# Performance work log

Measured on AMD Instinct MI355X. Metric: run time of the kernel, lower is better.

## Reference

```python
import jax, jax.numpy as jnp
import numpy as np

B, C, H, W = 4, 64, 64, 64  # x shape; mask is (B,1,8H,8W)


def _conv(x, w, pad=0):
    return jax.lax.conv_general_dilated(
        x, w, (1, 1), [(pad, pad), (pad, pad)],
        dimension_numbers=('NCHW', 'OIHW', 'NCHW'))


def _inorm(x, eps=1e-5):  # InstanceNorm2d, affine=False, biased var (torch default)
    mu = x.mean(axis=(2, 3), keepdims=True)
    var = x.var(axis=(2, 3), keepdims=True)
    return (x - mu) * jax.lax.rsqrt(var + eps)


def _forward(x, mask, kconv_w1, kconv_w2, fs_w1, fs_w2, fs_b2, fs_fuse_w):
    b, c, h, w = x.shape
    n = h * w
    # MaxPool2d(8,8) then binarize
    m = jax.lax.reduce_window(mask, -jnp.inf, jax.lax.max,
                              (1, 1, 8, 8), (1, 1, 8, 8), 'VALID')
    m = (m > 0).astype(x.dtype)
    back = 1.0 - m
    # ResidualBlock K_conv (shared for K and Q paths in original code)
    y = jax.nn.relu(_inorm(_conv(x, kconv_w1, pad=1)))
    y = _inorm(_conv(y, kconv_w2, pad=1))
    kx = jax.nn.relu(y + x)
    # L2-normalized K/Q over channel dim
    K = (kx * back).reshape(b, c, n)
    K = K / (jnp.linalg.norm(K, axis=1, keepdims=True) + 1e-8)
    Q = (kx * m).reshape(b, c, n)
    Q = Q / (jnp.linalg.norm(Q, axis=1, keepdims=True) + 1e-8)
    V = (x * back).reshape(b, c, n)
    # cosine-similarity score map, temperature 20
    score = jnp.einsum('bcq,bck->bqk', Q, K) * 20.0  # (b, n_q, n_k)
    qm = m.reshape(b, 1, n)      # query mask (foreground)
    km = back.reshape(b, 1, n)   # key mask (background)
    NEG = -1000000.0
    validx = score + (1.0 - km) * NEG + (1.0 - qm.transpose(0, 2, 1)) * NEG
    att = jax.nn.softmax(validx, axis=-1) * (qm.transpose(0, 2, 1) * km)
    # att_fore[b,c,q] = sum_k V[b,c,k] * att[b,q,k]
    att_fore = jnp.einsum('bck,bqk->bcq', V, att).reshape(b, c, h, w)
    # Fusion_score
    feat1 = _conv(jnp.concatenate([x * m, att_fore * m], axis=1), fs_w1)
    s = jax.nn.sigmoid(_conv(feat1, fs_w2) + fs_b2[None, :, None, None])
    fused = _conv(jnp.concatenate([x * m, att_fore * m * (1.0 - s)], axis=1), fs_fuse_w)
    fs_out = fused * m + x * (1.0 - m)
    out = fs_out * m + x * (1.0 - m)
    # visualization attention mask
    visatt = att.sum(axis=1).reshape(b, 1, h, w)
    attmask = jnp.repeat(jnp.repeat(visatt, 8, axis=2), 8, axis=3)  # nearest upsample x8
    attmask = attmask / attmask.max()
    return out, attmask


def setup_inputs() -> dict:
    key = jax.random.key(0)
    ks = jax.random.split(key, 8)

    def wgt(k, shape, fan_in):
        return jax.random.normal(k, shape, jnp.float32) / np.sqrt(fan_in)

    x = jax.random.normal(ks[0], (B, C, H, W), jnp.float32)
    # sparse foreground mask so maxpool(8x8)>0 yields a mixed fg/bg mask
    mask = (jax.random.uniform(ks[1], (B, 1, H * 8, W * 8)) < 0.01).astype(jnp.float32)
    return dict(
        x=x, mask=mask,
        kconv_w1=wgt(ks[2], (C, C, 3, 3), C * 9),
        kconv_w2=wgt(ks[3], (C, C, 3, 3), C * 9),
        fs_w1=wgt(ks[4], (C, 2 * C, 1, 1), 2 * C),
        fs_w2=wgt(ks[5], (C, C, 1, 1), C),
        fs_b2=jnp.zeros((C,), jnp.float32),
        fs_fuse_w=wgt(ks[6], (C, 2 * C, 1, 1), 2 * C),
    )


def reference(x, mask, kconv_w1, kconv_w2, fs_w1, fs_w2, fs_b2, fs_fuse_w):
    return _forward(x, mask, kconv_w1, kconv_w2, fs_w1, fs_w2, fs_b2, fs_fuse_w)
```

## Files before the change

### kernel.cpp

```cpp
#include <hip/hip_runtime.h>
#include <hip/hip_bf16.h>

typedef __hip_bfloat16 bf16;
typedef __attribute__((ext_vector_type(8))) short short8;
typedef __attribute__((ext_vector_type(4))) float f32x4;
typedef __attribute__((ext_vector_type(16))) float f32x16;

#define BB 4
#define CC 64
#define NN 4096
#define MH 512
#define MW 512
#define LS 72

#define WB_AFC  ((size_t)0)
#define WB_QIX  ((size_t)4325376)
#define WB_KIX  ((size_t)4390912)
#define WB_MFL  ((size_t)4456448)
#define WB_CNT  ((size_t)4472832)
#define WB_VIS  ((size_t)4259840)
#define WB_WT1  ((size_t)4476992)
#define WB_WT2  ((size_t)4550720)
#define WB_WFB  ((size_t)4624448)
#define WB_XT   ((size_t)8388608)
#define WB_KXT  ((size_t)10485760)
#define WB_E    ((size_t)16777216)
#define EB_ELEM ((size_t)16777216)
#define WB_AFCP ((size_t)150994944)
#define WB_DENP ((size_t)184549376)
#define WB_VISP ((size_t)185597952)
#define WB_GST  ((size_t)186122240)

__device__ __forceinline__ float us2f(unsigned short u) { return __uint_as_float(((unsigned)u) << 16); }
__device__ __forceinline__ unsigned short f2bu(float f) {
  bf16 h = __float2bfloat16(f);
  return *(unsigned short*)&h;
}

__global__ __launch_bounds__(256) void k_pre(const float* __restrict__ x,
                                             const float* __restrict__ mask,
                                             const float* __restrict__ w1,
                                             const float* __restrict__ w2,
                                             const float* __restrict__ fw1,
                                             const float* __restrict__ fw2,
                                             const float* __restrict__ fwf,
                                             float* __restrict__ outp,
                                             unsigned short* __restrict__ xt,
                                             unsigned char* __restrict__ mfl,
                                             float* __restrict__ vis,
                                             unsigned int* __restrict__ vmaxb,
                                             unsigned short* __restrict__ wT1,
                                             unsigned short* __restrict__ wT2,
                                             unsigned short* __restrict__ wfb) {
  __shared__ float lx[64][65];
  int t = threadIdx.x;
  if (blockIdx.x < 256) {
    int b = blockIdx.x >> 6, p0 = (blockIdx.x & 63) * 64;
    const float* xb = x + (size_t)b * CC * NN + p0;
    float* ob = outp + (size_t)b * CC * NN + p0;
    for (int idx = t; idx < 4096; idx += 256) {
      int c = idx >> 6, j = idx & 63;
      float v = xb[c * NN + j];
      lx[j][c] = v;
      ob[c * NN + j] = v;
    }
    __syncthreads();
    unsigned short* xo = xt + ((size_t)b * NN + p0) * 64;
    for (int idx = t; idx < 2048; idx += 256) {
      int j = idx >> 5, c2 = (idx & 31) * 2;
      ushort2 w2v;
      w2v.x = f2bu(lx[j][c2]);
      w2v.y = f2bu(lx[j][c2 + 1]);
      *(ushort2*)&xo[j * 64 + c2] = w2v;
    }
  } else {
    int g = (blockIdx.x - 256) * 256 + t;
    int o = g >> 2, sub = g & 3;
    int b = o >> 12, p = o & 4095;
    int py = p >> 6, px = p & 63;
    const float* mb = mask + (size_t)b * MH * MW + (py * 8 + sub * 2) * MW + px * 8;
    float mx = 0.f;
    #pragma unroll
    for (int dy = 0; dy < 2; ++dy) {
      const float4* r4 = (const float4*)(mb + dy * MW);
      float4 a = r4[0], c = r4[1];
      mx = fmaxf(mx, fmaxf(fmaxf(a.x, a.y), fmaxf(a.z, a.w)));
      mx = fmaxf(mx, fmaxf(fmaxf(c.x, c.y), fmaxf(c.z, c.w)));
    }
    mx = fmaxf(mx, __shfl_xor(mx, 1));
    mx = fmaxf(mx, __shfl_xor(mx, 2));
    if (sub == 0) {
      mfl[o] = (mx > 0.f) ? 1 : 0;
      vis[o] = 0.f;
    }
    if (g == 0) vmaxb[0] = 0u;
    if (g < 36864) {
      int tap = g >> 12;
      int rem = g & 4095;
      int co = rem >> 6, ci = rem & 63;
      int src = (co * 64 + ci) * 9 + tap;
      wT1[g] = f2bu(w1[src]);
      wT2[g] = f2bu(w2[src]);
    } else if (g < 57344) {
      int j2 = g - 36864;
      if (j2 < 8192)       wfb[j2] = f2bu(fw1[j2]);
      else if (j2 < 12288) wfb[j2] = f2bu(fw2[j2 - 8192]);
      else                 wfb[j2] = f2bu(fwf[j2 - 12288]);
    }
  }
}

__global__ __launch_bounds__(256) void k_compact(const unsigned char* __restrict__ mfl,
                                                 int* __restrict__ qidx, int* __restrict__ kidx,
                                                 int* __restrict__ nq, int* __restrict__ nk) {
  int b = blockIdx.x;
  __shared__ unsigned char lm[4096];
  int t = threadIdx.x;
  *(uint4*)&lm[t * 16] = *(const uint4*)&mfl[b * NN + t * 16];
  __syncthreads();
  if (t >= 64) return;
  int lane = t;
  int qb = 0, kb = 0;
  #pragma unroll
  for (int it = 0; it < 64; ++it) {
    int p = it * 64 + lane;
    bool f = lm[p] != 0;
    unsigned long long bal = __ballot(f);
    int before = __popcll(bal & ((1ULL << lane) - 1ULL));
    if (f)  qidx[b * NN + qb + before] = p;
    if (!f) kidx[b * NN + kb + (lane - before)] = p;
    int cnt = __popcll(bal);
    qb += cnt; kb += 64 - cnt;
  }
  if (lane == 0) { nq[b] = qb; nk[b] = kb; }
}

template <bool NORM_IN>
__global__ __launch_bounds__(256) void k_convm(const unsigned short* __restrict__ src,
                                               const unsigned short* __restrict__ wT,
                                               const float* __restrict__ insum,
                                               const float* __restrict__ insq,
                                               unsigned short* __restrict__ dst,
                                               float* __restrict__ gsump,
                                               float* __restrict__ gsqp) {
  int b = blockIdx.y;
  int r = blockIdx.x;
  __shared__ unsigned short bx[198 * LS];
  __shared__ float nmean[64], ninv[64];
  int t = threadIdx.x;
  if (NORM_IN) {
    if (t < 64) {
      float s = 0.f, s2v = 0.f;
      #pragma unroll 8
      for (int r2 = 0; r2 < 64; ++r2) {
        s   += insum[((size_t)r2 * BB + b) * 64 + t];
        s2v += insq [((size_t)r2 * BB + b) * 64 + t];
      }
      float m = s * (1.f / NN);
      float v = fmaxf(s2v * (1.f / NN) - m * m, 0.f);
      nmean[t] = m; ninv[t] = rsqrtf(v + 1e-5f);
    }
    __syncthreads();
  }
  const unsigned short* sb = src + (size_t)b * NN * 64;
  for (int idx = t; idx < 198 * 8; idx += 256) {
    int row = idx >> 3, c8 = (idx & 7) * 8;
    int dy = row / 66;
    int cx = row - dy * 66 - 1;
    int rr = r + dy - 1;
    uint4 v = make_uint4(0u, 0u, 0u, 0u);
    if ((unsigned)rr < 64u && (unsigned)cx < 64u) {
      v = *(const uint4*)(sb + ((size_t)(rr * 64 + cx)) * 64 + c8);
      if (NORM_IN) {
        unsigned short* e = (unsigned short*)&v;
        #pragma unroll
        for (int j = 0; j < 8; ++j)
          e[j] = f2bu(fmaxf((us2f(e[j]) - nmean[c8 + j]) * ninv[c8 + j], 0.f));
      }
    }
    *(uint4*)&bx[row * LS + c8] = v;
  }
  __syncthreads();
  int lane = t & 63;
  int quad = lane >> 4, col = lane & 15;
  int qw = (t >> 6) * 16;
  f32x4 acc[4] = {{0.f,0.f,0.f,0.f},{0.f,0.f,0.f,0.f},{0.f,0.f,0.f,0.f},{0.f,0.f,0.f,0.f}};
  #pragma unroll
  for (int tap = 0; tap < 9; ++tap) {
    int dy = tap / 3, dx = tap - dy * 3 - 1;
    const unsigned short* wrow = wT + ((size_t)tap * 64 + qw + col) * 64;
    short8 a0 = *(const short8*)(wrow + quad * 8);
    short8 a1 = *(const short8*)(wrow + 32 + quad * 8);
    int rbase = dy * 66 + dx + 1;
    #pragma unroll
    for (int nt = 0; nt < 4; ++nt) {
      int row = rbase + nt * 16 + col;
      short8 b0 = *(const short8*)&bx[row * LS + quad * 8];
      short8 b1 = *(const short8*)&bx[row * LS + 32 + quad * 8];
      acc[nt] = __builtin_amdgcn_mfma_f32_16x16x32_bf16(a0, b0, acc[nt], 0, 0, 0);
      acc[nt] = __builtin_amdgcn_mfma_f32_16x16x32_bf16(a1, b1, acc[nt], 0, 0, 0);
    }
  }
  #pragma unroll
  for (int rr = 0; rr < 4; ++rr) {
    float s1 = acc[0][rr] + acc[1][rr] + acc[2][rr] + acc[3][rr];
    float s2 = acc[0][rr]*acc[0][rr] + acc[1][rr]*acc[1][rr]
             + acc[2][rr]*acc[2][rr] + acc[3][rr]*acc[3][rr];
    s1 += __shfl_xor(s1, 1); s2 += __shfl_xor(s2, 1);
    s1 += __shfl_xor(s1, 2); s2 += __shfl_xor(s2, 2);
    s1 += __shfl_xor(s1, 4); s2 += __shfl_xor(s2, 4);
    s1 += __shfl_xor(s1, 8); s2 += __shfl_xor(s2, 8);
    if (col == 0) {
      int co = qw + quad * 4 + rr;
      gsump[((size_t)r * BB + b) * 64 + co] = s1;
      gsqp [((size_t)r * BB + b) * 64 + co] = s2;
    }
  }
  __syncthreads();
  #pragma unroll
  for (int nt = 0; nt < 4; ++nt)
    #pragma unroll
    for (int rr = 0; rr < 4; ++rr)
      bx[(nt * 16 + col) * LS + qw + quad * 4 + rr] = f2bu(acc[nt][rr]);
  __syncthreads();
  unsigned short* db = dst + ((size_t)b * NN + r * 64) * 64;
  for (int idx = t; idx < 512; idx += 256) {
    int px = idx >> 3, c8 = (idx & 7) * 8;
    *(uint4*)(db + (size_t)px * 64 + c8) = *(const uint4*)&bx[px * LS + c8];
  }
}

__global__ __launch_bounds__(256) void k_knorm(unsigned short* __restrict__ kxt,
                                               const unsigned short* __restrict__ xt,
                                               const float* __restrict__ gsump,
                                               const float* __restrict__ gsqp) {
  int b = blockIdx.x >> 6;
  int p0 = (blockIdx.x & 63) * 64;
  __shared__ float m2[64], i2[64];
  int t = threadIdx.x;
  if (t < 64) {
    float s = 0.f, s2v = 0.f;
    #pragma unroll 8
    for (int r2 = 0; r2 < 64; ++r2) {
      s   += gsump[((size_t)r2 * BB + b) * 64 + t];
      s2v += gsqp [((size_t)r2 * BB + b) * 64 + t];
    }
    float m = s * (1.f / NN);
    float v = fmaxf(s2v * (1.f / NN) - m * m, 0.f);
    m2[t] = m; i2[t] = rsqrtf(v + 1e-5f);
  }
  __syncthreads();
  int px = t >> 2, c0 = (t & 3) * 16;
  size_t base = ((size_t)b * NN + p0 + px) * 64 + c0;
  unsigned short kv[16], xv[16];
  *(uint4*)&kv[0] = *(const uint4*)(kxt + base);
  *(uint4*)&kv[8] = *(const uint4*)(kxt + base + 8);
  *(uint4*)&xv[0] = *(const uint4*)(xt + base);
  *(uint4*)&xv[8] = *(const uint4*)(xt + base + 8);
  float v[16]; float ss = 0.f;
  #pragma unroll
  for (int j = 0; j < 16; ++j) {
    float f = fmaxf((us2f(kv[j]) - m2[c0 + j]) * i2[c0 + j] + us2f(xv[j]), 0.f);
    v[j] = f; ss += f * f;
  }
  ss += __shfl_xor(ss, 1);
  ss += __shfl_xor(ss, 2);
  float inv = 1.f / (sqrtf(ss) + 1e-8f);
  #pragma unroll
  for (int j = 0; j < 16; ++j) kv[j] = f2bu(v[j] * inv);
  *(uint4*)(kxt + base) = *(const uint4*)&kv[0];
  *(uint4*)(kxt + base + 8) = *(const uint4*)&kv[8];
}

__global__ __launch_bounds__(256) void k_att1(const unsigned short* __restrict__ khat,
                                              const unsigned short* __restrict__ xt,
                                              const int* __restrict__ qidx, const int* __restrict__ kidx,
                                              const int* __restrict__ nqv, const int* __restrict__ nkv,
                                              float* __restrict__ afc_part, float* __restrict__ den_part,
                                              unsigned short* __restrict__ eg) {
  int b = blockIdx.y;
  int nqb = nqv[b], nkb = nkv[b];
  int q0 = (blockIdx.x >> 3) * 64;
  int part = blockIdx.x & 7;
  if (q0 >= nqb) return;
  int ntiles = (nkb + 63) >> 6;
  int nt_blk = (part < ntiles) ? ((ntiles - part + 7) >> 3) : 0;
  int NKP = (nkb + 63) & ~63;
  __shared__ unsigned short lk [64 * LS];
  __shared__ unsigned short lvT[64 * LS];
  __shared__ unsigned short le [64 * LS];
  __shared__ int lidxa[512];
  int t = threadIdx.x;
  int wave = t >> 6, lane = t & 63;
  int l31 = lane & 31, lhi = lane >> 5;
  int qh = wave >> 1, kh = wave & 1;
  const int* qix = qidx + b * NN;
  const int* kix = kidx + b * NN;
  const unsigned short* khb = khat + (size_t)b * NN * 64;
  const unsigned short* xtb = xt + (size_t)b * NN * 64;
  unsigned short* egb = eg + (size_t)b * EB_ELEM;
  float* afcp = afc_part + (((size_t)part * BB + b) * NN) * 64;
  float* denp = den_part + (((size_t)(part * 2 + kh)) * BB + b) * NN;
  int qq_a = q0 + qh * 32 + l31;
  int qp_a = (qq_a < nqb) ? qix[qq_a] : qix[0];
  short8 aq[4];
  #pragma unroll
  for (int ks = 0; ks < 4; ++ks)
    aq[ks] = *(const short8*)(khb + (size_t)qp_a * 64 + ks * 16 + lhi * 8);
  for (int idx = t; idx < nt_blk * 64; idx += 256) {
    int it = idx >> 6, k = idx & 63;
    lidxa[idx] = kix[(part + it * 8) * 64 + k];
  }
  __syncthreads();
  int klo = t >> 3, c8 = (t & 7) * 8, vcc = t & 7;
  uint4 g0, g1, g2, g3;
  auto issue_gather = [&](int it) {
    int j0 = (part + it * 8) * 64;
    const int* lp = lidxa + it * 64;
    uint4 z = make_uint4(0u, 0u, 0u, 0u);
    g0 = (j0 + klo      < nkb) ? *(const uint4*)(khb + (size_t)lp[klo] * 64 + c8) : z;
    g1 = (j0 + klo + 32 < nkb) ? *(const uint4*)(khb + (size_t)lp[klo + 32] * 64 + c8) : z;
    g2 = (j0 + 2 * klo     < nkb) ? *(const uint4*)(xtb + (size_t)lp[2 * klo] * 64 + c8) : z;
    g3 = (j0 + 2 * klo + 1 < nkb) ? *(const uint4*)(xtb + (size_t)lp[2 * klo + 1] * 64 + c8) : z;
  };
  if (nt_blk > 0) issue_gather(0);
  f32x16 pv, dsum;
  #pragma unroll
  for (int i = 0; i < 16; ++i) { pv[i] = 0.f; dsum[i] = 0.f; }
  for (int it = 0; it < nt_blk; ++it) {
    int j0 = (part + it * 8) * 64;
    __syncthreads();
    *(uint4*)&lk[klo * LS + c8] = g0;
    *(uint4*)&lk[(klo + 32) * LS + c8] = g1;
    {
      const unsigned short* e0 = (const unsigned short*)&g2;
      const unsigned short* e1 = (const unsigned short*)&g3;
      int pbase = klo & 3, prun = klo >> 2;
      int pp = pbase + ((prun ^ vcc) << 2);
      #pragma unroll
      for (int jj = 0; jj < 8; ++jj) {
        unsigned int w2 = (unsigned)e0[jj] | ((unsigned)e1[jj] << 16);
        *(unsigned int*)&lvT[(c8 + jj) * LS + pp * 2] = w2;
      }
    }
    __syncthreads();
    if (it + 1 < nt_blk) issue_gather(it + 1);
    f32x16 s;
    #pragma unroll
    for (int i = 0; i < 16; ++i) s[i] = 0.f;
    #pragma unroll
    for (int ks = 0; ks < 4; ++ks) {
      short8 bk = *(const short8*)&lk[(kh * 32 + l31) * LS + ks * 16 + lhi * 8];
      s = __builtin_amdgcn_mfma_f32_32x32x16_bf16(aq[ks], bk, s, 0, 0, 0);
    }
    bool kval = (j0 + kh * 32 + l31) < nkb;
    #pragma unroll
    for (int reg = 0; reg < 16; ++reg) {
      float e = kval ? __expf(20.f * s[reg]) : 0.f;
      dsum[reg] += e;
      int row = (reg & 3) + 8 * (reg >> 2) + 4 * lhi;
      le[(qh * 32 + row) * LS + kh * 32 + l31] = f2bu(e);
    }
    __syncthreads();
    for (int idx = t; idx < 512; idx += 256) {
      int q = idx >> 3, cc8 = (idx & 7) * 8;
      if (q0 + q < nqb)
        *(uint4*)(egb + (size_t)(q0 + q) * NKP + j0 + cc8) = *(const uint4*)&le[q * LS + cc8];
    }
    int c = kh * 32 + l31;
    int c37 = (c >> 3) & 7;
    #pragma unroll
    for (int ks = 0; ks < 4; ++ks) {
      short8 a  = *(const short8*)&le[(qh * 32 + l31) * LS + ks * 16 + lhi * 8];
      int run = ks * 2 + lhi;
      short8 bv = *(const short8*)&lvT[c * LS + ((run ^ c37) << 3)];
      pv = __builtin_amdgcn_mfma_f32_32x32x16_bf16(a, bv, pv, 0, 0, 0);
    }
  }
  #pragma unroll
  for (int reg = 0; reg < 16; ++reg) {
    float v = dsum[reg];
    v += __shfl_xor(v, 1); v += __shfl_xor(v, 2); v += __shfl_xor(v, 4);
    v += __shfl_xor(v, 8); v += __shfl_xor(v, 16);
    int row = (reg & 3) + 8 * (reg >> 2) + 4 * lhi;
    int qq = q0 + qh * 32 + row;
    if (l31 == 0 && qq < nqb) denp[qq] = v;
  }
  #pragma unroll
  for (int reg = 0; reg < 16; ++reg) {
    int row = (reg & 3) + 8 * (reg >> 2) + 4 * lhi;
    int qq = q0 + qh * 32 + row;
    if (qq < nqb) afcp[(size_t)qq * 64 + kh * 32 + l31] = pv[reg];
  }
}

__global__ __launch_bounds__(256) void k_vis(const unsigned short* __restrict__ eg,
                                             const float* __restrict__ den_part,
                                             const int* __restrict__ nqv, const int* __restrict__ nkv,
                                             float* __restrict__ visp) {
  int b = blockIdx.z;
  int nqb = nqv[b], nkb = nkv[b];
  int k0 = blockIdx.x * 256;
  if (k0 >= nkb) return;
  int NKP = (nkb + 63) & ~63;
  int qpart = blockIdx.y;
  int qbeg = (qpart * nqb) >> 3;
  int qend = ((qpart + 1) * nqb) >> 3;
  __shared__ float wd[256];
  int t = threadIdx.x;
  int k = k0 + t;
  const unsigned short* eb = eg + (size_t)b * EB_ELEM;
  float acc = 0.f;
  for (int qc = qbeg; qc < qend; qc += 256) {
    __syncthreads();
    int qq = qc + t;
    float d = 0.f;
    if (qq < qend) {
      #pragma unroll
      for (int p2 = 0; p2 < 16; ++p2) d += den_part[((size_t)p2 * BB + b) * NN + qq];
    }
    wd[t] = (d > 0.f) ? 1.f / d : 0.f;
    __syncthreads();
    int lim = min(256, qend - qc);
    if (k < nkb) {
      const unsigned short* ep = eb + (size_t)qc * NKP + k;
      int j = 0;
      for (; j + 8 <= lim; j += 8) {
        #pragma unroll
        for (int u = 0; u < 8; ++u)
          acc += us2f(ep[(size_t)(j + u) * NKP]) * wd[j + u];
      }
      for (; j < lim; ++j)
        acc += us2f(ep[(size_t)j * NKP]) * wd[j];
    }
  }
  if (k < nkb) visp[((size_t)qpart * BB + b) * NN + k] = acc;
}

#define FS 136
__global__ __launch_bounds__(256) void k_fusionm(const unsigned short* __restrict__ xt,
                                                 const float* __restrict__ afc_part,
                                                 const float* __restrict__ den_part,
                                                 const int* __restrict__ qidx, const int* __restrict__ nqv,
                                                 const unsigned short* __restrict__ wall,
                                                 const float* __restrict__ b2,
                                                 float* __restrict__ outp) {
  int b = blockIdx.y;
  int nqb = nqv[b];
  int q0 = blockIdx.x * 64;
  if (q0 >= nqb) return;
  __shared__ unsigned short pxa[64 * FS];
  __shared__ unsigned short f1s[64 * LS];
  __shared__ int qpl[64];
  int t = threadIdx.x;
  int lane = t & 63;
  int quad = lane >> 4, col = lane & 15;
  int cb = (t >> 6) * 16;
  const int* qix = qidx + b * NN;
  const unsigned short* xtb = xt + (size_t)b * NN * 64;
  const unsigned short* w1b = wall;
  const unsigned short* w2b = wall + 8192;
  const unsigned short* wfb = wall + 12288;
  short8 a1[4], a2[2], af[4];
  #pragma unroll
  for (int kt = 0; kt < 4; ++kt) {
    a1[kt] = *(const short8*)&w1b[(cb + col) * 128 + kt * 32 + quad * 8];
    af[kt] = *(const short8*)&wfb[(cb + col) * 128 + kt * 32 + quad * 8];
  }
  #pragma unroll
  for (int kt = 0; kt < 2; ++kt)
    a2[kt] = *(const short8*)&w2b[(cb + col) * 64 + kt * 32 + quad * 8];
  float b2v[4];
  #pragma unroll
  for (int r = 0; r < 4; ++r) b2v[r] = b2[cb + quad * 4 + r];
  if (t < 64) qpl[t] = (q0 + t < nqb) ? qix[q0 + t] : -1;
  for (int idx = t; idx < 512; idx += 256) {
    int q = idx >> 3, c8 = (idx & 7) * 8;
    int qq = q0 + q;
    uint4 pv = make_uint4(0u, 0u, 0u, 0u);
    unsigned short pa8[8] = {0, 0, 0, 0, 0, 0, 0, 0};
    if (qq < nqb) {
      int qp = qix[qq];
      pv = *(const uint4*)(xtb + (size_t)qp * 64 + c8);
      float d = 0.f;
      #pragma unroll
      for (int p2 = 0; p2 < 16; ++p2)
        d += den_part[((size_t)p2 * BB + b) * NN + qq];
      float av[8];
      #pragma unroll
      for (int j = 0; j < 8; ++j) av[j] = 0.f;
      #pragma unroll
      for (int p2 = 0; p2 < 8; ++p2) {
        const float4* ap4 = (const float4*)(afc_part + (((size_t)p2 * BB + b) * NN + qq) * 64 + c8);
        float4 u0 = ap4[0], u1 = ap4[1];
        av[0] += u0.x; av[1] += u0.y; av[2] += u0.z; av[3] += u0.w;
        av[4] += u1.x; av[5] += u1.y; av[6] += u1.z; av[7] += u1.w;
      }
      float invd = (d > 0.f) ? 1.f / d : 0.f;
      #pragma unroll
      for (int j = 0; j < 8; ++j) pa8[j] = f2bu(av[j] * invd);
    }
    *(uint4*)&pxa[q * FS + c8] = pv;
    *(uint4*)&pxa[q * FS + 64 + c8] = *(const uint4*)&pa8[0];
  }
  __syncthreads();
  #pragma unroll
  for (int qt = 0; qt < 4; ++qt) {
    f32x4 acc = {0.f, 0.f, 0.f, 0.f};
    #pragma unroll
    for (int kt = 0; kt < 4; ++kt) {
      short8 bfrag = *(const short8*)&pxa[(qt * 16 + col) * FS + kt * 32 + quad * 8];
      acc = __builtin_amdgcn_mfma_f32_16x16x32_bf16(a1[kt], bfrag, acc, 0, 0, 0);
    }
    #pragma unroll
    for (int r = 0; r < 4; ++r)
      f1s[(qt * 16 + col) * LS + cb + quad * 4 + r] = f2bu(acc[r]);
  }
  __syncthreads();
  #pragma unroll
  for (int qt = 0; qt < 4; ++qt) {
    f32x4 acc = {0.f, 0.f, 0.f, 0.f};
    #pragma unroll
    for (int kt = 0; kt < 2; ++kt) {
      short8 bfrag = *(const short8*)&f1s[(qt * 16 + col) * LS + kt * 32 + quad * 8];
      acc = __builtin_amdgcn_mfma_f32_16x16x32_bf16(a2[kt], bfrag, acc, 0, 0, 0);
    }
    #pragma unroll
    for (int r = 0; r < 4; ++r) {
      float sg = 1.f / (1.f + __expf(-(acc[r] + b2v[r])));
      int addr = (qt * 16 + col) * FS + 64 + cb + quad * 4 + r;
      pxa[addr] = f2bu(us2f(pxa[addr]) * (1.f - sg));
    }
  }
  __syncthreads();
  #pragma unroll
  for (int qt = 0; qt < 4; ++qt) {
    f32x4 acc = {0.f, 0.f, 0.f, 0.f};
    #pragma unroll
    for (int kt = 0; kt < 4; ++kt) {
      short8 bfrag = *(const short8*)&pxa[(qt * 16 + col) * FS + kt * 32 + quad * 8];
      acc = __builtin_amdgcn_mfma_f32_16x16x32_bf16(af[kt], bfrag, acc, 0, 0, 0);
    }
    int qp = qpl[qt * 16 + col];
    if (qp >= 0) {
      #pragma unroll
      for (int r = 0; r < 4; ++r)
        outp[((size_t)b * CC + cb + quad * 4 + r) * NN + qp] = acc[r];
    }
  }
}

__global__ __launch_bounds__(256) void k_vmax(const float* __restrict__ visp,
                                              const int* __restrict__ kidx,
                                              const int* __restrict__ nkv,
                                              float* __restrict__ vis,
                                              unsigned int* __restrict__ vmaxb) {
  int i = blockIdx.x * 256 + threadIdx.x;
  int b = i >> 12, k = i & 4095;
  float v = 0.f;
  if (k < nkv[b]) {
    #pragma unroll
    for (int p2 = 0; p2 < 8; ++p2) v += visp[((size_t)p2 * BB + b) * NN + k];
    vis[b * NN + kidx[b * NN + k]] = v;
  }
  #pragma unroll
  for (int off = 32; off > 0; off >>= 1) v = fmaxf(v, __shfl_down(v, off));
  if ((threadIdx.x & 63) == 0) atomicMax(vmaxb, __float_as_uint(v));
}

__global__ __launch_bounds__(256) void k_upsample(const float* __restrict__ vis,
                                                  const unsigned int* __restrict__ vmaxb,
                                                  float* __restrict__ out2) {
  int i4 = blockIdx.x * 256 + threadIdx.x;
  int b = i4 >> 16;
  int rem = i4 & 65535;
  int y = rem >> 7, x4 = (rem & 127) * 4;
  float vm = __uint_as_float(vmaxb[0]);
  if (!(vm > 0.f)) vm = 1.f;
  float v = vis[b * NN + (y >> 3) * 64 + (x4 >> 3)] / vm;
  ((float4*)out2)[i4] = make_float4(v, v, v, v);
}

extern "C" void kernel_launch(void* const* d_in, const int* in_sizes, int n_in,
                              void* d_out, int out_size, void* d_ws, size_t ws_size,
                              hipStream_t stream) {
  const float* x    = (const float*)d_in[0];
  const float* mask = (const float*)d_in[1];
  const float* w1   = (const float*)d_in[2];
  const float* w2c  = (const float*)d_in[3];
  const float* fsw1 = (const float*)d_in[4];
  const float* fsw2 = (const float*)d_in[5];
  const float* fsb2 = (const float*)d_in[6];
  const float* fswf = (const float*)d_in[7];
  float* out = (float*)d_out;
  char* wsb = (char*)d_ws;

  float* vis = (float*)(wsb + WB_VIS);
  int* qidx  = (int*)(wsb + WB_QIX);
  int* kidx  = (int*)(wsb + WB_KIX);
  unsigned char* mfl = (unsigned char*)(wsb + WB_MFL);
  int* nq = (int*)(wsb + WB_CNT);
  int* nk = nq + 4;
  unsigned int* vmaxb = (unsigned int*)(nq + 8);
  unsigned short* wT1 = (unsigned short*)(wsb + WB_WT1);
  unsigned short* wT2 = (unsigned short*)(wsb + WB_WT2);
  unsigned short* wall = (unsigned short*)(wsb + WB_WFB);
  unsigned short* y1t = (unsigned short*)(wsb + WB_AFC);
  unsigned short* xt  = (unsigned short*)(wsb + WB_XT);
  unsigned short* kxt = (unsigned short*)(wsb + WB_KXT);
  unsigned short* khat = kxt;
  unsigned short* eg  = (unsigned short*)(wsb + WB_E);
  float* afc_part = (float*)(wsb + WB_AFCP);
  float* den_part = (float*)(wsb + WB_DENP);
  float* visp     = (float*)(wsb + WB_VISP);
  float* gsum1p = (float*)(wsb + WB_GST);
  float* gsq1p  = (float*)(wsb + WB_GST + 65536);
  float* gsum2p = (float*)(wsb + WB_GST + 131072);
  float* gsq2p  = (float*)(wsb + WB_GST + 196608);

  k_pre<<<512, 256, 0, stream>>>(x, mask, w1, w2c, fsw1, fsw2, fswf,
                                 out, xt, mfl, vis, vmaxb, wT1, wT2, wall);
  k_compact<<<4, 256, 0, stream>>>(mfl, qidx, kidx, nq, nk);
  k_convm<false><<<dim3(64, BB), 256, 0, stream>>>(xt, wT1, nullptr, nullptr, y1t, gsum1p, gsq1p);
  k_convm<true><<<dim3(64, BB), 256, 0, stream>>>(y1t, wT2, gsum1p, gsq1p, kxt, gsum2p, gsq2p);
  k_knorm<<<256, 256, 0, stream>>>(kxt, xt, gsum2p, gsq2p);
  k_att1<<<dim3(512, BB), 256, 0, stream>>>(khat, xt, qidx, kidx, nq, nk, afc_part, den_part, eg);
  k_vis<<<dim3(16, 8, BB), 256, 0, stream>>>(eg, den_part, nq, nk, visp);
  k_fusionm<<<dim3(64, BB), 256, 0, stream>>>(xt, afc_part, den_part, qidx, nq, wall, fsb2, out);
  k_vmax<<<64, 256, 0, stream>>>(visp, kidx, nk, vis, vmaxb);
  k_upsample<<<1024, 256, 0, stream>>>(vis, vmaxb, out + 1048576);
}
```

Measured before the change: 174.6 us.

## Pre-gather compacted K/V/Q rows and double key-split partitions in attention

Adds a gather kernel that writes the foreground queries and background keys/values into contiguous compacted buffers, so the attention kernel reads rows sequentially instead of going through index indirection. The attention kernel also splits the key dimension into 16 parts instead of 8, which doubles the grid for more parallelism. The cost is an extra launch, extra workspace traffic, and twice as many partial sums for afc and den that the fusion and vis kernels must reduce.

```diff
diff --git a/kernel.cpp b/kernel.cpp
--- a/kernel.cpp
+++ b/kernel.cpp
@@ -12,24 +12,29 @@
 #define MH 512
 #define MW 512
 #define LS 72
+#define NPARTS 16
+#define NDEN 32
 
 #define WB_AFC  ((size_t)0)
+#define WB_VIS  ((size_t)4259840)
 #define WB_QIX  ((size_t)4325376)
 #define WB_KIX  ((size_t)4390912)
 #define WB_MFL  ((size_t)4456448)
 #define WB_CNT  ((size_t)4472832)
-#define WB_VIS  ((size_t)4259840)
 #define WB_WT1  ((size_t)4476992)
 #define WB_WT2  ((size_t)4550720)
 #define WB_WFB  ((size_t)4624448)
+#define WB_KC   ((size_t)5242880)
 #define WB_XT   ((size_t)8388608)
 #define WB_KXT  ((size_t)10485760)
+#define WB_VC   ((size_t)12582912)
+#define WB_QC   ((size_t)14680064)
 #define WB_E    ((size_t)16777216)
 #define EB_ELEM ((size_t)16777216)
 #define WB_AFCP ((size_t)150994944)
-#define WB_DENP ((size_t)184549376)
-#define WB_VISP ((size_t)185597952)
-#define WB_GST  ((size_t)186122240)
+#define WB_DENP ((size_t)218103808)
+#define WB_VISP ((size_t)220200960)
+#define WB_GST  ((size_t)220725248)
 
 __device__ __forceinline__ float us2f(unsigned short u) { return __uint_as_float(((unsigned)u) << 16); }
 __device__ __forceinline__ unsigned short f2bu(float f) {
@@ -272,63 +277,90 @@
   *(uint4*)(kxt + base + 8) = *(const uint4*)&kv[8];
 }
 
-__global__ __launch_bounds__(256) void k_att1(const unsigned short* __restrict__ khat,
+__global__ __launch_bounds__(256) void k_gath(const unsigned short* __restrict__ khat,
                                               const unsigned short* __restrict__ xt,
                                               const int* __restrict__ qidx, const int* __restrict__ kidx,
+                                              const int* __restrict__ nqv, const int* __restrict__ nkv,
+                                              unsigned short* __restrict__ kc,
+                                              unsigned short* __restrict__ vc,
+                                              unsigned short* __restrict__ qc) {
+  int b = blockIdx.y;
+  int j0 = blockIdx.x * 64;
+  int nqb = nqv[b], nkb = nkv[b];
+  int NKP = (nkb + 63) & ~63, NQP = (nqb + 63) & ~63;
+  bool dok = j0 < NKP, doq = j0 < NQP;
+  if (!dok && !doq) return;
+  __shared__ int li[128];
+  int t = threadIdx.x;
+  if (t < 64)       li[t]      = (j0 + t < nkb) ? kidx[b * NN + j0 + t] : -1;
+  else if (t < 128) li[t - 64 + 64] = li[t - 64 + 64];
+  if (t >= 64 && t < 128) li[t] = (j0 + (t - 64) < nqb) ? qidx[b * NN + j0 + (t - 64)] : -1;
+  __syncthreads();
+  const unsigned short* khb = khat + (size_t)b * NN * 64;
+  const unsigned short* xtb = xt + (size_t)b * NN * 64;
+  uint4 z = make_uint4(0u, 0u, 0u, 0u);
+  for (int idx = t; idx < 512; idx += 256) {
+    int row = idx >> 3, c8 = (idx & 7) * 8;
+    size_t dsto = ((size_t)b * NN + j0 + row) * 64 + c8;
+    if (dok) {
+      int sk = li[row];
+      *(uint4*)(kc + dsto) = (sk >= 0) ? *(const uint4*)(khb + (size_t)sk * 64 + c8) : z;
+      *(uint4*)(vc + dsto) = (sk >= 0) ? *(const uint4*)(xtb + (size_t)sk * 64 + c8) : z;
+    }
+    if (doq) {
+      int sq = li[64 + row];
+      *(uint4*)(qc + dsto) = (sq >= 0) ? *(const uint4*)(khb + (size_t)sq * 64 + c8) : z;
+    }
+  }
+}
+
+__global__ __launch_bounds__(256) void k_att1(const unsigned short* __restrict__ kc,
+                                              const unsigned short* __restrict__ vc,
+                                              const unsigned short* __restrict__ qc,
                                               const int* __restrict__ nqv, const int* __restrict__ nkv,
                                               float* __restrict__ afc_part, float* __restrict__ den_part,
                                               unsigned short* __restrict__ eg) {
   int b = blockIdx.y;
   int nqb = nqv[b], nkb = nkv[b];
-  int q0 = (blockIdx.x >> 3) * 64;
-  int part = blockIdx.x & 7;
+  int q0 = (blockIdx.x >> 4) * 64;
+  int part = blockIdx.x & (NPARTS - 1);
   if (q0 >= nqb) return;
   int ntiles = (nkb + 63) >> 6;
-  int nt_blk = (part < ntiles) ? ((ntiles - part + 7) >> 3) : 0;
+  int nt_blk = (part < ntiles) ? ((ntiles - part + NPARTS - 1) >> 4) : 0;
   int NKP = (nkb + 63) & ~63;
   __shared__ unsigned short lk [64 * LS];
   __shared__ unsigned short lvT[64 * LS];
   __shared__ unsigned short le [64 * LS];
-  __shared__ int lidxa[512];
   int t = threadIdx.x;
   int wave = t >> 6, lane = t & 63;
   int l31 = lane & 31, lhi = lane >> 5;
   int qh = wave >> 1, kh = wave & 1;
-  const int* qix = qidx + b * NN;
-  const int* kix = kidx + b * NN;
-  const unsigned short* khb = khat + (size_t)b * NN * 64;
-  const unsigned short* xtb = xt + (size_t)b * NN * 64;
+  const unsigned short* kcb = kc + (size_t)b * NN * 64;
+  const unsigned short* vcb = vc + (size_t)b * NN * 64;
+  const unsigned short* qcb = qc + (size_t)b * NN * 64;
   unsigned short* egb = eg + (size_t)b * EB_ELEM;
   float* afcp = afc_part + (((size_t)part * BB + b) * NN) * 64;
   float* denp = den_part + (((size_t)(part * 2 + kh)) * BB + b) * NN;
   int qq_a = q0 + qh * 32 + l31;
-  int qp_a = (qq_a < nqb) ? qix[qq_a] : qix[0];
   short8 aq[4];
   #pragma unroll
   for (int ks = 0; ks < 4; ++ks)
-    aq[ks] = *(const short8*)(khb + (size_t)qp_a * 64 + ks * 16 + lhi * 8);
-  for (int idx = t; idx < nt_blk * 64; idx += 256) {
-    int it = idx >> 6, k = idx & 63;
-    lidxa[idx] = kix[(part + it * 8) * 64 + k];
-  }
-  __syncthreads();
+    aq[ks] = *(const short8*)(qcb + (size_t)qq_a * 64 + ks * 16 + lhi * 8);
   int klo = t >> 3, c8 = (t & 7) * 8, vcc = t & 7;
   uint4 g0, g1, g2, g3;
   auto issue_gather = [&](int it) {
-    int j0 = (part + it * 8) * 64;
-    const int* lp = lidxa + it * 64;
-    uint4 z = make_uint4(0u, 0u, 0u, 0u);
-    g0 = (j0 + klo      < nkb) ? *(const uint4*)(khb + (size_t)lp[klo] * 64 + c8) : z;
-    g1 = (j0 + klo + 32 < nkb) ? *(const uint4*)(khb + (size_t)lp[klo + 32] * 64 + c8) : z;
-    g2 = (j0 + 2 * klo     < nkb) ? *(const uint4*)(xtb + (size_t)lp[2 * klo] * 64 + c8) : z;
-    g3 = (j0 + 2 * klo + 1 < nkb) ? *(const uint4*)(xtb + (size_t)lp[2 * klo + 1] * 64 + c8) : z;
+    int j0 = (part + it * NPARTS) * 64;
+    g0 = *(const uint4*)(kcb + (size_t)(j0 + klo) * 64 + c8);
+    g1 = *(const uint4*)(kcb + (size_t)(j0 + klo + 32) * 64 + c8);
+    g2 = *(const uint4*)(vcb + (size_t)(j0 + 2 * klo) * 64 + c8);
+    g3 = *(const uint4*)(vcb + (size_t)(j0 + 2 * klo + 1) * 64 + c8);
   };
   if (nt_blk > 0) issue_gather(0);
   f32x16 pv, dsum;
   #pragma unroll
   for (int i = 0; i < 16; ++i) { pv[i] = 0.f; dsum[i] = 0.f; }
   for (int it = 0; it < nt_blk; ++it) {
-    int j0 = (part + it * 8) * 64;
+    int j0 = (part + it * NPARTS) * 64;
     __syncthreads();
     *(uint4*)&lk[klo * LS + c8] = g0;
     *(uint4*)&lk[(klo + 32) * LS + c8] = g1;
@@ -417,7 +449,7 @@
     float d = 0.f;
     if (qq < qend) {
       #pragma unroll
-      for (int p2 = 0; p2 < 16; ++p2) d += den_part[((size_t)p2 * BB + b) * NN + qq];
+      for (int p2 = 0; p2 < NDEN; ++p2) d += den_part[((size_t)p2 * BB + b) * NN + qq];
     }
     wd[t] = (d > 0.f) ? 1.f / d : 0.f;
     __syncthreads();
@@ -484,13 +516,13 @@
       pv = *(const uint4*)(xtb + (size_t)qp * 64 + c8);
       float d = 0.f;
       #pragma unroll
-      for (int p2 = 0; p2 < 16; ++p2)
+      for (int p2 = 0; p2 < NDEN; ++p2)
         d += den_part[((size_t)p2 * BB + b) * NN + qq];
       float av[8];
       #pragma unroll
       for (int j = 0; j < 8; ++j) av[j] = 0.f;
       #pragma unroll
-      for (int p2 = 0; p2 < 8; ++p2) {
+      for (int p2 = 0; p2 < NPARTS; ++p2) {
         const float4* ap4 = (const float4*)(afc_part + (((size_t)p2 * BB + b) * NN + qq) * 64 + c8);
         float4 u0 = ap4[0], u1 = ap4[1];
         av[0] += u0.x; av[1] += u0.y; av[2] += u0.z; av[3] += u0.w;
@@ -609,6 +641,9 @@
   unsigned short* xt  = (unsigned short*)(wsb + WB_XT);
   unsigned short* kxt = (unsigned short*)(wsb + WB_KXT);
   unsigned short* khat = kxt;
+  unsigned short* kc  = (unsigned short*)(wsb + WB_KC);
+  unsigned short* vc  = (unsigned short*)(wsb + WB_VC);
+  unsigned short* qc  = (unsigned short*)(wsb + WB_QC);
   unsigned short* eg  = (unsigned short*)(wsb + WB_E);
   float* afc_part = (float*)(wsb + WB_AFCP);
   float* den_part = (float*)(wsb + WB_DENP);
@@ -624,7 +659,8 @@
   k_convm<false><<<dim3(64, BB), 256, 0, stream>>>(xt, wT1, nullptr, nullptr, y1t, gsum1p, gsq1p);
   k_convm<true><<<dim3(64, BB), 256, 0, stream>>>(y1t, wT2, gsum1p, gsq1p, kxt, gsum2p, gsq2p);
   k_knorm<<<256, 256, 0, stream>>>(kxt, xt, gsum2p, gsq2p);
-  k_att1<<<dim3(512, BB), 256, 0, stream>>>(khat, xt, qidx, kidx, nq, nk, afc_part, den_part, eg);
+  k_gath<<<dim3(64, BB), 256, 0, stream>>>(khat, xt, qidx, kidx, nq, nk, kc, vc, qc);
+  k_att1<<<dim3(64 * NPARTS, BB), 256, 0, stream>>>(kc, vc, qc, nq, nk, afc_part, den_part, eg);
   k_vis<<<dim3(16, 8, BB), 256, 0, stream>>>(eg, den_part, nq, nk, visp);
   k_fusionm<<<dim3(64, BB), 256, 0, stream>>>(xt, afc_part, den_part, qidx, nq, wall, fsb2, out);
   k_vmax<<<64, 256, 0, stream>>>(visp, kidx, nk, vis, vmaxb);
```

Measured after the change: 175.8 us. No clear change (+0.7%).
